# Kernel optimization log

Hardware: AMD Instinct MI355X
Metric: run time of the kernel (lower is better)

Reference implementation:

```python
import jax, jax.numpy as jnp
import numpy as np

NUM_ATOMS = 50000
NUM_EDGES = 200000  # even: edges come in (fwd, rev) pairs
D_V, D_E, D_H = 133, 14, 256
DEPTH = 3


def setup_inputs() -> dict:
    key = jax.random.key(0)
    ks = jax.random.split(key, 12)
    half = NUM_EDGES // 2
    src = jax.random.randint(ks[0], (half,), 0, NUM_ATOMS)
    dst = jax.random.randint(ks[1], (half,), 0, NUM_ATOMS)
    v = jnp.concatenate([src, dst])
    w = jnp.concatenate([dst, src])
    edge_index = jnp.stack([v, w])  # [2, E]
    rev_edge_index = jnp.concatenate([jnp.arange(half) + half, jnp.arange(half)])

    def lin(k, out_d, in_d):
        return jax.random.normal(k, (out_d, in_d), jnp.float32) / np.sqrt(in_d)

    return {
        "V": jax.random.normal(ks[2], (NUM_ATOMS, D_V), jnp.float32),
        "E_feat": jax.random.normal(ks[3], (NUM_EDGES, D_E), jnp.float32),
        "edge_index": edge_index,
        "rev_edge_index": rev_edge_index,
        "Wi_atom": lin(ks[4], D_H, D_V),
        "Wi_bond": lin(ks[5], D_H, D_V + D_E),
        "Wh_atom": lin(ks[6], D_H, D_H),
        "Wh_bond": lin(ks[7], D_H, D_H),
        "Wf_atom": lin(ks[8], D_H, D_H),
        "Wf_bond": lin(ks[9], D_H, D_H),
        "Wo_atom": lin(ks[10], D_H, D_V + D_H),
    }


def _sum_and_max_into_atoms(H_e, w_idx, num_atoms):
    a_sum = jax.ops.segment_sum(H_e, w_idx, num_segments=num_atoms)
    a_max = jax.ops.segment_max(H_e, w_idx, num_segments=num_atoms)
    a_max = jnp.where(jnp.isfinite(a_max), a_max, 0.0)  # empty segments -> 0
    return a_sum, a_max


def _fuse(H, m, Wf):
    # Fusion(kind='mlp', residual=True), dropout=0:
    # residual update with a small MLP on the combined signal
    return H + jax.nn.relu((H + m) @ Wf.T)


def reference(V, E_feat, edge_index, rev_edge_index, Wi_atom, Wi_bond,
              Wh_atom, Wh_bond, Wf_atom, Wf_bond, Wo_atom):
    tau = jax.nn.relu
    num_atoms = V.shape[0]
    v = edge_index[0]
    w = edge_index[1]

    H_a = tau(V @ Wi_atom.T)                                        # [N, d_h]
    H_b = tau(jnp.concatenate([V[v], E_feat], axis=1) @ Wi_bond.T)  # [E, d_h]

    for _ in range(1, DEPTH):
        a_sum, a_max = _sum_and_max_into_atoms(H_b, w, num_atoms)
        gate = a_sum * a_max
        m_a = gate @ Wh_atom.T
        H_a = _fuse(H_a, m_a, Wf_atom)

        M_b = a_sum[v] - H_b[rev_edge_index]
        m_b = M_b @ Wh_bond.T
        H_b = _fuse(H_b, m_b, Wf_bond)

    a_sum, _ = _sum_and_max_into_atoms(H_b, w, num_atoms)
    H_atom = tau(jnp.concatenate([V, a_sum], axis=1) @ Wo_atom.T)   # [N, d_h]
    return H_atom
```

## Files before the change

kernel.cpp:

```cpp
#include <hip/hip_runtime.h>
#include <hip/hip_bf16.h>

#define NATOM 50000
#define NEDGE 200000
#define HALF  100000
#define DV    133
#define DE    14
#define DH    256
#define KVP   160
#define NBLK_SCAN ((NATOM + 255) / 256)

typedef __bf16  bf16x8 __attribute__((ext_vector_type(8)));
typedef __bf16  bf16x4 __attribute__((ext_vector_type(4)));
typedef float   f32x4  __attribute__((ext_vector_type(4)));

__device__ __forceinline__ void gll16(const void* g, void* l) {
    __builtin_amdgcn_global_load_lds(
        (const __attribute__((address_space(1))) unsigned int*)g,
        (__attribute__((address_space(3))) unsigned int*)l, 16, 0, 0);
}
__device__ __forceinline__ void drain_barrier() {
    __builtin_amdgcn_s_waitcnt(0);
    __syncthreads();
}
__device__ __forceinline__ int swz(int row, int byteInRow) {
    return row * 512 + (byteInRow ^ ((row & 7) << 4));
}


struct DArgs {
    const float* Vf; const float* Ef; const float* asumf;
    const int* vidx;
    const __bf16* W1; const __bf16* W2;
    __bf16* C; float* Cf;
    int M;
};

template<int MODE, int KITERS>
__global__ __launch_bounds__(512, 4) void dgemm(DArgs g) {
    const int tid = threadIdx.x;
    const int lane = tid & 63, wv = tid >> 6;
    const int quad = lane >> 4, l16 = lane & 15;
    const int wr = (wv >> 2) * 64, wc = (wv & 3) * 64;
    const int gr0 = blockIdx.x * 128;

    int vrow[4]; const float* epp[4];
#pragma unroll
    for (int m = 0; m < 4; ++m) {
        int r = gr0 + wr + m * 16 + l16;
        if (r > g.M - 1) r = g.M - 1;
        vrow[m] = (MODE == 1) ? g.vidx[r] : r;
        epp[m] = (MODE == 1) ? (g.Ef + (size_t)r * DE) : nullptr;
    }

    f32x4 acc[16];
#pragma unroll
    for (int i = 0; i < 16; ++i) acc[i] = (f32x4){0.f, 0.f, 0.f, 0.f};

#pragma unroll
    for (int kk = 0; kk < KITERS; ++kk) {
        bf16x8 af[4];
#pragma unroll
        for (int m = 0; m < 4; ++m) {
            const int cb = kk * 32 + quad * 8;
            if (MODE != 2 || kk < 5) {
                const float* vp = g.Vf + (size_t)vrow[m] * DV;
                if (kk < 4) {
                    f32x4 x0, x1;
                    __builtin_memcpy(&x0, vp + cb, 16);
                    __builtin_memcpy(&x1, vp + cb + 4, 16);
#pragma unroll
                    for (int j = 0; j < 4; ++j) {
                        af[m][j] = (__bf16)x0[j]; af[m][4 + j] = (__bf16)x1[j];
                    }
                } else {
#pragma unroll
                    for (int j = 0; j < 8; ++j) {
                        int c = cb + j; float y = 0.f;
                        if (c < DV) y = vp[c];
                        else if (MODE == 1 && c < DV + DE) y = epp[m][c - DV];
                        af[m][j] = (__bf16)y;
                    }
                }
            } else {
                const float* sp = g.asumf + (size_t)vrow[m] * DH + (kk - 5) * 32 + quad * 8;
                f32x4 s0 = *(const f32x4*)sp, s1 = *(const f32x4*)(sp + 4);
#pragma unroll
                for (int j = 0; j < 4; ++j) {
                    af[m][j] = (__bf16)s0[j]; af[m][4 + j] = (__bf16)s1[j];
                }
            }
        }
        bf16x8 bfv[4];
#pragma unroll
        for (int n = 0; n < 4; ++n) {
            int col = wc + n * 16 + l16;
            const __bf16* wp;
            if (MODE == 2 && kk >= 5) wp = g.W2 + (size_t)col * DH  + (kk - 5) * 32 + quad * 8;
            else                      wp = g.W1 + (size_t)col * KVP + kk * 32 + quad * 8;
            bfv[n] = *(const bf16x8*)wp;
        }
#pragma unroll
        for (int m = 0; m < 4; ++m)
#pragma unroll
            for (int n = 0; n < 4; ++n)
                acc[m * 4 + n] = __builtin_amdgcn_mfma_f32_16x16x32_bf16(
                    af[m], bfv[n], acc[m * 4 + n], 0, 0, 0);
    }

#pragma unroll
    for (int m = 0; m < 4; ++m)
#pragma unroll
    for (int n = 0; n < 4; ++n)
#pragma unroll
    for (int r = 0; r < 4; ++r) {
        int gr = gr0 + wr + m * 16 + quad * 4 + r;
        if (gr < g.M) {
            int col = wc + n * 16 + l16;
            float v = acc[m * 4 + n][r];
            v = v > 0.f ? v : 0.f;
            if (MODE == 2) g.Cf[(size_t)gr * DH + col] = v;
            else           g.C [(size_t)gr * DH + col] = (__bf16)v;
        }
    }
}

struct FArgs {
    const float* asumf; const __bf16* asumb; const __bf16* amaxb;
    const int* vidx;
    const __bf16* W1; const __bf16* W2;
    __bf16* H;
    int M;
};

template<int BOND>
__global__ __launch_bounds__(512, 2) void fgemm(FArgs g) {
    __shared__ __bf16 Hlds[32768];
    __shared__ __bf16 Tlds[32768];
    const int tid = threadIdx.x;
    const int lane = tid & 63, wv = tid >> 6;
    const int quad = lane >> 4, l16 = lane & 15;
    const int wr = (wv >> 2) * 64, wc = (wv & 3) * 64;
    const int bid = blockIdx.x;

#pragma unroll
    for (int it = 0; it < 8; ++it) {
        int unit = it * 512 + wv * 64 + lane;
        int lr = unit >> 5, u16 = unit & 31;
        int srow;
        if (BOND) {
            int sl = bid * 64 + (lr & 63); if (sl > g.M - 1) sl = g.M - 1;
            srow = (lr < 64) ? sl : g.M + sl;
        } else {
            srow = bid * 128 + lr; if (srow > g.M - 1) srow = g.M - 1;
        }
        const char* src = (const char*)g.H + (size_t)srow * 512
                        + ((u16 * 16) ^ ((lr & 7) << 4));
        gll16(src, (char*)Hlds + it * 8192 + wv * 1024);
    }

    int garow[4];
#pragma unroll
    for (int m = 0; m < 4; ++m) {
        int lr = wr + m * 16 + l16;
        if (BOND) {
            int sl = bid * 64 + (lr & 63); if (sl > g.M - 1) sl = g.M - 1;
            int gA = (lr < 64) ? sl : g.M + sl;
            garow[m] = g.vidx[gA];
        } else {
            int r = bid * 128 + lr; if (r > g.M - 1) r = g.M - 1;
            garow[m] = r;
        }
    }

    f32x4 acc[16];
#pragma unroll
    for (int i = 0; i < 16; ++i) acc[i] = (f32x4){0.f, 0.f, 0.f, 0.f};

    drain_barrier();

#pragma unroll
    for (int kk = 0; kk < 8; ++kk) {
        const int cb = kk * 32 + quad * 8;
        const int byC = cb * 2;
        bf16x8 af[4];
#pragma unroll
        for (int m = 0; m < 4; ++m) {
            int lr = wr + m * 16 + l16;
            if (BOND) {
                bf16x8 a = *(const bf16x8*)(g.asumb + (size_t)garow[m] * DH + cb);
                int lrH = lr ^ 64;
                bf16x8 h = *(const bf16x8*)((const char*)Hlds + swz(lrH, byC));
#pragma unroll
                for (int j = 0; j < 8; ++j)
                    af[m][j] = (__bf16)((float)a[j] - (float)h[j]);
            } else {
                const float* s = g.asumf + (size_t)garow[m] * DH + cb;
                f32x4 s0 = *(const f32x4*)s, s1 = *(const f32x4*)(s + 4);
                bf16x8 mx = *(const bf16x8*)(g.amaxb + (size_t)garow[m] * DH + cb);
#pragma unroll
                for (int j = 0; j < 4; ++j) {
                    af[m][j]     = (__bf16)(s0[j] * (float)mx[j]);
                    af[m][4 + j] = (__bf16)(s1[j] * (float)mx[4 + j]);
                }
            }
        }
        bf16x8 bfv[4];
#pragma unroll
        for (int n = 0; n < 4; ++n)
            bfv[n] = *(const bf16x8*)(g.W1 + (size_t)(wc + n * 16 + l16) * DH + cb);
#pragma unroll
        for (int m = 0; m < 4; ++m)
#pragma unroll
            for (int n = 0; n < 4; ++n)
                acc[m * 4 + n] = __builtin_amdgcn_mfma_f32_16x16x32_bf16(
                    af[m], bfv[n], acc[m * 4 + n], 0, 0, 0);
    }

#pragma unroll
    for (int m = 0; m < 4; ++m)
#pragma unroll
    for (int n = 0; n < 4; ++n)
#pragma unroll
    for (int r = 0; r < 4; ++r) {
        int lr = wr + m * 16 + quad * 4 + r;
        int col = wc + n * 16 + l16;
        float b = (float)*(const __bf16*)((const char*)Hlds + swz(lr, col * 2));
        *(__bf16*)((char*)Tlds + swz(lr, col * 2)) = (__bf16)(b + acc[m * 4 + n][r]);
    }
    drain_barrier();

#pragma unroll
    for (int i = 0; i < 16; ++i) acc[i] = (f32x4){0.f, 0.f, 0.f, 0.f};
#pragma unroll
    for (int kk = 0; kk < 8; ++kk) {
        bf16x8 af[4], bfv[4];
#pragma unroll
        for (int m = 0; m < 4; ++m) {
            int lr = wr + m * 16 + l16;
            af[m] = *(const bf16x8*)((const char*)Tlds + swz(lr, kk * 64 + quad * 16));
        }
#pragma unroll
        for (int n = 0; n < 4; ++n)
            bfv[n] = *(const bf16x8*)(g.W2 + (size_t)(wc + n * 16 + l16) * DH + kk * 32 + quad * 8);
#pragma unroll
        for (int m = 0; m < 4; ++m)
#pragma unroll
            for (int n = 0; n < 4; ++n)
                acc[m * 4 + n] = __builtin_amdgcn_mfma_f32_16x16x32_bf16(
                    af[m], bfv[n], acc[m * 4 + n], 0, 0, 0);
    }

#pragma unroll
    for (int m = 0; m < 4; ++m)
#pragma unroll
    for (int n = 0; n < 4; ++n)
#pragma unroll
    for (int r = 0; r < 4; ++r) {
        int lr = wr + m * 16 + quad * 4 + r;
        int col = wc + n * 16 + l16;
        int off = swz(lr, col * 2);
        float b = (float)*(const __bf16*)((const char*)Hlds + off);
        float v = acc[m * 4 + n][r];
        v = v > 0.f ? v : 0.f;
        *(__bf16*)((char*)Hlds + off) = (__bf16)(b + v);
    }
    drain_barrier();

#pragma unroll
    for (int it = 0; it < 8; ++it) {
        int unit = it * 512 + tid;
        int lr = unit >> 5, u16 = unit & 31;
        bool ok; int srow;
        if (BOND) {
            int sl = bid * 64 + (lr & 63); ok = sl < g.M;
            srow = (lr < 64) ? sl : g.M + sl;
        } else {
            srow = bid * 128 + lr; ok = srow < g.M;
        }
        if (ok) {
            bf16x8 v = *(const bf16x8*)((const char*)Hlds
                        + swz(lr, u16 * 16));
            *(bf16x8*)((char*)g.H + (size_t)srow * 512 + u16 * 16) = v;
        }
    }
}

__global__ void count_deg(const int* __restrict__ widx, int* __restrict__ cnt) {
    int e = blockIdx.x * 256 + threadIdx.x;
    if (e < NEDGE) atomicAdd(&cnt[widx[e]], 1);
}

__global__ __launch_bounds__(256) void scan_p1(const int* __restrict__ cnt,
                                               int* __restrict__ rowptr,
                                               int* __restrict__ bsum) {
    __shared__ int sm[256];
    const int tid = threadIdx.x;
    const int i = blockIdx.x * 256 + tid;
    int v = (i < NATOM) ? cnt[i] : 0;
    sm[tid] = v;
    __syncthreads();
    for (int off = 1; off < 256; off <<= 1) {
        int t = (tid >= off) ? sm[tid - off] : 0;
        __syncthreads();
        sm[tid] += t;
        __syncthreads();
    }
    if (i < NATOM) rowptr[i] = sm[tid] - v;
    if (tid == 255) bsum[blockIdx.x] = sm[255];
}

__global__ __launch_bounds__(256) void scan_p2(int* __restrict__ bsum) {
    __shared__ int sm[256];
    const int tid = threadIdx.x;
    int v = (tid < NBLK_SCAN) ? bsum[tid] : 0;
    sm[tid] = v;
    __syncthreads();
    for (int off = 1; off < 256; off <<= 1) {
        int t = (tid >= off) ? sm[tid - off] : 0;
        __syncthreads();
        sm[tid] += t;
        __syncthreads();
    }
    if (tid < NBLK_SCAN) bsum[tid] = sm[tid] - v;
    if (tid == 255) bsum[NBLK_SCAN] = sm[255];
}

__global__ __launch_bounds__(256) void scan_p3(int* __restrict__ rowptr,
                                               int* __restrict__ cursor,
                                               const int* __restrict__ bsum) {
    const int i = blockIdx.x * 256 + threadIdx.x;
    if (i < NATOM) {
        int r = rowptr[i] + bsum[blockIdx.x];
        rowptr[i] = r;
        cursor[i] = r;
    }
    if (i == 0) rowptr[NATOM] = bsum[NBLK_SCAN];
}

__global__ void fill_csr(const int* __restrict__ widx, int* __restrict__ cursor,
                         int* __restrict__ eid) {
    int e = blockIdx.x * 256 + threadIdx.x;
    if (e >= NEDGE) return;
    int pos = atomicAdd(&cursor[widx[e]], 1);
    eid[pos] = e;
}

template<int WITHMAX>
__global__ __launch_bounds__(256) void seg_reduce(
    const __bf16* __restrict__ Hb, const int* __restrict__ rowptr,
    const int* __restrict__ eid,
    float* __restrict__ asum, __bf16* __restrict__ asumb,
    __bf16* __restrict__ amaxb)
{
    int a = blockIdx.x * 4 + (threadIdx.x >> 6);
    if (a >= NATOM) return;
    const int lane = threadIdx.x & 63;
    const int beg = rowptr[a], end = rowptr[a + 1];
    float s0 = 0.f, s1 = 0.f, s2 = 0.f, s3 = 0.f;
    float m0 = 0.f, m1 = 0.f, m2 = 0.f, m3 = 0.f;
    for (int i = beg; i < end; ++i) {
        int e = eid[i];
        bf16x4 h = *(const bf16x4*)(Hb + (size_t)e * DH + lane * 4);
        float v0 = (float)h[0], v1 = (float)h[1], v2 = (float)h[2], v3 = (float)h[3];
        s0 += v0; s1 += v1; s2 += v2; s3 += v3;
        if (WITHMAX) {
            m0 = fmaxf(m0, v0); m1 = fmaxf(m1, v1);
            m2 = fmaxf(m2, v2); m3 = fmaxf(m3, v3);
        }
    }
    size_t o = (size_t)a * DH + lane * 4;
    *(f32x4*)(asum + o) = (f32x4){s0, s1, s2, s3};
    if (WITHMAX) {
        bf16x4 sv; sv[0] = (__bf16)s0; sv[1] = (__bf16)s1; sv[2] = (__bf16)s2; sv[3] = (__bf16)s3;
        *(bf16x4*)(asumb + o) = sv;
        bf16x4 mv; mv[0] = (__bf16)m0; mv[1] = (__bf16)m1; mv[2] = (__bf16)m2; mv[3] = (__bf16)m3;
        *(bf16x4*)(amaxb + o) = mv;
    }
}

__global__ void pad_w2(const float* __restrict__ src, __bf16* __restrict__ dst,
                       int srcld, int coloff, int KS, int KD) {
    int i = blockIdx.x * 256 + threadIdx.x;
    if (i >= 256 * KD) return;
    int n = i / KD, c = i - n * KD;
    dst[i] = (c < KS) ? (__bf16)src[(size_t)n * srcld + coloff + c] : (__bf16)0.f;
}

static inline int cdiv(long a, long b) { return (int)((a + b - 1) / b); }

extern "C" void kernel_launch(void* const* d_in, const int* in_sizes, int n_in,
                              void* d_out, int out_size, void* d_ws, size_t ws_size,
                              hipStream_t stream) {
    const float* V    = (const float*)d_in[0];
    const float* Ef   = (const float*)d_in[1];
    const int*   ei   = (const int*)d_in[2];
    const int*   rev  = (const int*)d_in[3];
    const float* Wi_a = (const float*)d_in[4];
    const float* Wi_b = (const float*)d_in[5];
    const float* Wh_a = (const float*)d_in[6];
    const float* Wh_b = (const float*)d_in[7];
    const float* Wf_a = (const float*)d_in[8];
    const float* Wf_b = (const float*)d_in[9];
    const float* Wo   = (const float*)d_in[10];
    float* out = (float*)d_out;
    (void)rev;

    const int* vidx = ei;
    const int* widx = ei + NEDGE;

    char* ws = (char*)d_ws;
    __bf16* Hb    = (__bf16*)(ws + 0);
    __bf16* Ha    = (__bf16*)(ws + 102400000);
    float*  asum  = (float*) (ws + 128000000);
    __bf16* asumb = (__bf16*)(ws + 179200000);
    __bf16* amaxb = (__bf16*)(ws + 204800000);
    __bf16* Wia   = (__bf16*)(ws + 230400000);
    __bf16* Wib   = (__bf16*)(ws + 230481920);
    __bf16* Wo1   = (__bf16*)(ws + 230563840);
    __bf16* Wo2   = (__bf16*)(ws + 230645760);
    __bf16* Wha   = (__bf16*)(ws + 230776832);
    __bf16* Whb   = (__bf16*)(ws + 230907904);
    __bf16* Wfa   = (__bf16*)(ws + 231038976);
    __bf16* Wfb   = (__bf16*)(ws + 231170048);
    int*  rowptr  = (int*)(ws + 231301120);
    int*  cursor  = (int*)(ws + 231501312);
    int*  eid     = (int*)(ws + 231701504);
    int*  bsum    = (int*)(ws + 232501504);
    (void)ws_size;

    hipMemsetAsync(cursor, 0, NATOM * sizeof(int), stream);
    count_deg<<<cdiv(NEDGE, 256), 256, 0, stream>>>(widx, cursor);
    scan_p1<<<NBLK_SCAN, 256, 0, stream>>>(cursor, rowptr, bsum);
    scan_p2<<<1, 256, 0, stream>>>(bsum);
    scan_p3<<<NBLK_SCAN, 256, 0, stream>>>(rowptr, cursor, bsum);
    fill_csr<<<cdiv(NEDGE, 256), 256, 0, stream>>>(widx, cursor, eid);

    pad_w2<<<cdiv(256 * KVP, 256), 256, 0, stream>>>(Wi_a, Wia, DV, 0, DV, KVP);
    pad_w2<<<cdiv(256 * KVP, 256), 256, 0, stream>>>(Wi_b, Wib, DV + DE, 0, DV + DE, KVP);
    pad_w2<<<cdiv(256 * KVP, 256), 256, 0, stream>>>(Wo, Wo1, DV + DH, 0, DV, KVP);
    pad_w2<<<cdiv(256 * DH, 256), 256, 0, stream>>>(Wo, Wo2, DV + DH, DV, DH, DH);
    pad_w2<<<cdiv(256 * DH, 256), 256, 0, stream>>>(Wh_a, Wha, DH, 0, DH, DH);
    pad_w2<<<cdiv(256 * DH, 256), 256, 0, stream>>>(Wh_b, Whb, DH, 0, DH, DH);
    pad_w2<<<cdiv(256 * DH, 256), 256, 0, stream>>>(Wf_a, Wfa, DH, 0, DH, DH);
    pad_w2<<<cdiv(256 * DH, 256), 256, 0, stream>>>(Wf_b, Wfb, DH, 0, DH, DH);

    {
        DArgs d{}; d.Vf = V; d.W1 = Wia; d.C = Ha; d.M = NATOM;
        dgemm<0, 5><<<cdiv(NATOM, 128), 512, 0, stream>>>(d);
    }
    {
        DArgs d{}; d.Vf = V; d.Ef = Ef; d.vidx = vidx; d.W1 = Wib; d.C = Hb; d.M = NEDGE;
        dgemm<1, 5><<<cdiv(NEDGE, 128), 512, 0, stream>>>(d);
    }

    for (int it = 0; it < 2; ++it) {
        seg_reduce<1><<<cdiv(NATOM, 4), 256, 0, stream>>>(Hb, rowptr, eid, asum, asumb, amaxb);
        {
            FArgs f{}; f.asumf = asum; f.amaxb = amaxb;
            f.W1 = Wha; f.W2 = Wfa; f.H = Ha; f.M = NATOM;
            fgemm<0><<<cdiv(NATOM, 128), 512, 0, stream>>>(f);
        }
        {
            FArgs f{}; f.asumb = asumb; f.vidx = vidx;
            f.W1 = Whb; f.W2 = Wfb; f.H = Hb; f.M = HALF;
            fgemm<1><<<cdiv(HALF, 64), 512, 0, stream>>>(f);
        }
    }

    seg_reduce<0><<<cdiv(NATOM, 4), 256, 0, stream>>>(Hb, rowptr, eid, asum, nullptr, nullptr);
    {
        DArgs d{}; d.Vf = V; d.asumf = asum; d.W1 = Wo1; d.W2 = Wo2; d.Cf = out; d.M = NATOM;
        dgemm<2, 13><<<cdiv(NATOM, 128), 512, 0, stream>>>(d);
    }
}
```

Before: 1.089 ms.

## Halve fgemm row tile, swap MFMA operands, prefetch gathered asum rows

```diff
diff --git a/kernel.cpp b/kernel.cpp
--- a/kernel.cpp
+++ b/kernel.cpp
@@ -134,153 +134,158 @@
 };
 
 template<int BOND>
-__global__ __launch_bounds__(512, 2) void fgemm(FArgs g) {
-    __shared__ __bf16 Hlds[32768];
-    __shared__ __bf16 Tlds[32768];
+__global__ __launch_bounds__(512, 4) void fgemm(FArgs g) {
+    __shared__ __bf16 Hlds[16384];
+    __shared__ __bf16 Tlds[16384];
     const int tid = threadIdx.x;
     const int lane = tid & 63, wv = tid >> 6;
     const int quad = lane >> 4, l16 = lane & 15;
-    const int wr = (wv >> 2) * 64, wc = (wv & 3) * 64;
+    const int wr = (wv >> 2) * 32;
+    const int wc = (wv & 3) * 64;
     const int bid = blockIdx.x;
 
-#pragma unroll
-    for (int it = 0; it < 8; ++it) {
+    int garow[2];
+#pragma unroll
+    for (int fr = 0; fr < 2; ++fr) {
+        int lr = wr + fr * 16 + l16;
+        if (BOND) {
+            int sl = bid * 32 + (lr & 31);
+            int gA = (lr < 32) ? sl : HALF + sl;
+            garow[fr] = g.vidx[gA];
+        } else {
+            int r = bid * 64 + lr; if (r > g.M - 1) r = g.M - 1;
+            garow[fr] = r;
+        }
+    }
+    bf16x8 pf[2][8];
+    if (BOND) {
+#pragma unroll
+        for (int fr = 0; fr < 2; ++fr)
+#pragma unroll
+        for (int kk = 0; kk < 8; ++kk)
+            pf[fr][kk] = *(const bf16x8*)(g.asumb + (size_t)garow[fr] * DH
+                                          + kk * 32 + quad * 8);
+    }
+
+#pragma unroll
+    for (int it = 0; it < 4; ++it) {
         int unit = it * 512 + wv * 64 + lane;
         int lr = unit >> 5, u16 = unit & 31;
         int srow;
-        if (BOND) {
-            int sl = bid * 64 + (lr & 63); if (sl > g.M - 1) sl = g.M - 1;
-            srow = (lr < 64) ? sl : g.M + sl;
-        } else {
-            srow = bid * 128 + lr; if (srow > g.M - 1) srow = g.M - 1;
-        }
+        if (BOND) { int sl = bid * 32 + (lr & 31); srow = (lr < 32) ? sl : HALF + sl; }
+        else      { srow = bid * 64 + lr; if (srow > g.M - 1) srow = g.M - 1; }
         const char* src = (const char*)g.H + (size_t)srow * 512
                         + ((u16 * 16) ^ ((lr & 7) << 4));
         gll16(src, (char*)Hlds + it * 8192 + wv * 1024);
     }
-
-    int garow[4];
-#pragma unroll
-    for (int m = 0; m < 4; ++m) {
-        int lr = wr + m * 16 + l16;
-        if (BOND) {
-            int sl = bid * 64 + (lr & 63); if (sl > g.M - 1) sl = g.M - 1;
-            int gA = (lr < 64) ? sl : g.M + sl;
-            garow[m] = g.vidx[gA];
-        } else {
-            int r = bid * 128 + lr; if (r > g.M - 1) r = g.M - 1;
-            garow[m] = r;
-        }
-    }
-
-    f32x4 acc[16];
-#pragma unroll
-    for (int i = 0; i < 16; ++i) acc[i] = (f32x4){0.f, 0.f, 0.f, 0.f};
-
     drain_barrier();
+
+    f32x4 acc[8];
+#pragma unroll
+    for (int i = 0; i < 8; ++i) acc[i] = (f32x4){0.f, 0.f, 0.f, 0.f};
 
 #pragma unroll
     for (int kk = 0; kk < 8; ++kk) {
         const int cb = kk * 32 + quad * 8;
-        const int byC = cb * 2;
-        bf16x8 af[4];
-#pragma unroll
-        for (int m = 0; m < 4; ++m) {
-            int lr = wr + m * 16 + l16;
+        bf16x8 mf[2];
+#pragma unroll
+        for (int fr = 0; fr < 2; ++fr) {
+            int lr = wr + fr * 16 + l16;
             if (BOND) {
-                bf16x8 a = *(const bf16x8*)(g.asumb + (size_t)garow[m] * DH + cb);
-                int lrH = lr ^ 64;
-                bf16x8 h = *(const bf16x8*)((const char*)Hlds + swz(lrH, byC));
+                bf16x8 h = *(const bf16x8*)((const char*)Hlds + swz(lr ^ 32, cb * 2));
 #pragma unroll
                 for (int j = 0; j < 8; ++j)
-                    af[m][j] = (__bf16)((float)a[j] - (float)h[j]);
+                    mf[fr][j] = (__bf16)((float)pf[fr][kk][j] - (float)h[j]);
             } else {
-                const float* s = g.asumf + (size_t)garow[m] * DH + cb;
+                const float* s = g.asumf + (size_t)garow[fr] * DH + cb;
                 f32x4 s0 = *(const f32x4*)s, s1 = *(const f32x4*)(s + 4);
-                bf16x8 mx = *(const bf16x8*)(g.amaxb + (size_t)garow[m] * DH + cb);
+                bf16x8 mx = *(const bf16x8*)(g.amaxb + (size_t)garow[fr] * DH + cb);
 #pragma unroll
                 for (int j = 0; j < 4; ++j) {
-                    af[m][j]     = (__bf16)(s0[j] * (float)mx[j]);
-                    af[m][4 + j] = (__bf16)(s1[j] * (float)mx[4 + j]);
+                    mf[fr][j]     = (__bf16)(s0[j] * (float)mx[j]);
+                    mf[fr][4 + j] = (__bf16)(s1[j] * (float)mx[4 + j]);
                 }
             }
         }
-        bf16x8 bfv[4];
-#pragma unroll
-        for (int n = 0; n < 4; ++n)
-            bfv[n] = *(const bf16x8*)(g.W1 + (size_t)(wc + n * 16 + l16) * DH + cb);
-#pragma unroll
-        for (int m = 0; m < 4; ++m)
-#pragma unroll
-            for (int n = 0; n < 4; ++n)
-                acc[m * 4 + n] = __builtin_amdgcn_mfma_f32_16x16x32_bf16(
-                    af[m], bfv[n], acc[m * 4 + n], 0, 0, 0);
-    }
-
-#pragma unroll
-    for (int m = 0; m < 4; ++m)
-#pragma unroll
-    for (int n = 0; n < 4; ++n)
-#pragma unroll
-    for (int r = 0; r < 4; ++r) {
-        int lr = wr + m * 16 + quad * 4 + r;
-        int col = wc + n * 16 + l16;
-        float b = (float)*(const __bf16*)((const char*)Hlds + swz(lr, col * 2));
-        *(__bf16*)((char*)Tlds + swz(lr, col * 2)) = (__bf16)(b + acc[m * 4 + n][r]);
+        bf16x8 wf[4];
+#pragma unroll
+        for (int fc = 0; fc < 4; ++fc)
+            wf[fc] = *(const bf16x8*)(g.W1 + (size_t)(wc + fc * 16 + l16) * DH + cb);
+#pragma unroll
+        for (int fc = 0; fc < 4; ++fc)
+#pragma unroll
+            for (int fr = 0; fr < 2; ++fr)
+                acc[fc * 2 + fr] = __builtin_amdgcn_mfma_f32_16x16x32_bf16(
+                    wf[fc], mf[fr], acc[fc * 2 + fr], 0, 0, 0);
+    }
+
+#pragma unroll
+    for (int fc = 0; fc < 4; ++fc)
+#pragma unroll
+    for (int fr = 0; fr < 2; ++fr) {
+        int row = wr + fr * 16 + l16;
+        int colb = wc + fc * 16 + quad * 4;
+        int off = swz(row, colb * 2);
+        bf16x4 h = *(const bf16x4*)((const char*)Hlds + off);
+        bf16x4 t;
+#pragma unroll
+        for (int j = 0; j < 4; ++j)
+            t[j] = (__bf16)((float)h[j] + acc[fc * 2 + fr][j]);
+        *(bf16x4*)((char*)Tlds + off) = t;
     }
     drain_barrier();
 
 #pragma unroll
-    for (int i = 0; i < 16; ++i) acc[i] = (f32x4){0.f, 0.f, 0.f, 0.f};
+    for (int i = 0; i < 8; ++i) acc[i] = (f32x4){0.f, 0.f, 0.f, 0.f};
 #pragma unroll
     for (int kk = 0; kk < 8; ++kk) {
-        bf16x8 af[4], bfv[4];
-#pragma unroll
-        for (int m = 0; m < 4; ++m) {
-            int lr = wr + m * 16 + l16;
-            af[m] = *(const bf16x8*)((const char*)Tlds + swz(lr, kk * 64 + quad * 16));
-        }
-#pragma unroll
-        for (int n = 0; n < 4; ++n)
-            bfv[n] = *(const bf16x8*)(g.W2 + (size_t)(wc + n * 16 + l16) * DH + kk * 32 + quad * 8);
-#pragma unroll
-        for (int m = 0; m < 4; ++m)
-#pragma unroll
-            for (int n = 0; n < 4; ++n)
-                acc[m * 4 + n] = __builtin_amdgcn_mfma_f32_16x16x32_bf16(
-                    af[m], bfv[n], acc[m * 4 + n], 0, 0, 0);
-    }
-
-#pragma unroll
-    for (int m = 0; m < 4; ++m)
-#pragma unroll
-    for (int n = 0; n < 4; ++n)
-#pragma unroll
-    for (int r = 0; r < 4; ++r) {
-        int lr = wr + m * 16 + quad * 4 + r;
-        int col = wc + n * 16 + l16;
-        int off = swz(lr, col * 2);
-        float b = (float)*(const __bf16*)((const char*)Hlds + off);
-        float v = acc[m * 4 + n][r];
-        v = v > 0.f ? v : 0.f;
-        *(__bf16*)((char*)Hlds + off) = (__bf16)(b + v);
+        const int cb = kk * 32 + quad * 8;
+        bf16x8 tf[2];
+#pragma unroll
+        for (int fr = 0; fr < 2; ++fr) {
+            int lr = wr + fr * 16 + l16;
+            tf[fr] = *(const bf16x8*)((const char*)Tlds + swz(lr, cb * 2));
+        }
+        bf16x8 wf[4];
+#pragma unroll
+        for (int fc = 0; fc < 4; ++fc)
+            wf[fc] = *(const bf16x8*)(g.W2 + (size_t)(wc + fc * 16 + l16) * DH + cb);
+#pragma unroll
+        for (int fc = 0; fc < 4; ++fc)
+#pragma unroll
+            for (int fr = 0; fr < 2; ++fr)
+                acc[fc * 2 + fr] = __builtin_amdgcn_mfma_f32_16x16x32_bf16(
+                    wf[fc], tf[fr], acc[fc * 2 + fr], 0, 0, 0);
+    }
+
+#pragma unroll
+    for (int fc = 0; fc < 4; ++fc)
+#pragma unroll
+    for (int fr = 0; fr < 2; ++fr) {
+        int row = wr + fr * 16 + l16;
+        int colb = wc + fc * 16 + quad * 4;
+        int off = swz(row, colb * 2);
+        bf16x4 h = *(const bf16x4*)((const char*)Hlds + off);
+        bf16x4 o;
+#pragma unroll
+        for (int j = 0; j < 4; ++j) {
+            float v = acc[fc * 2 + fr][j];
+            v = v > 0.f ? v : 0.f;
+            o[j] = (__bf16)((float)h[j] + v);
+        }
+        *(bf16x4*)((char*)Hlds + off) = o;
     }
     drain_barrier();
 
 #pragma unroll
-    for (int it = 0; it < 8; ++it) {
+    for (int it = 0; it < 4; ++it) {
         int unit = it * 512 + tid;
         int lr = unit >> 5, u16 = unit & 31;
         bool ok; int srow;
-        if (BOND) {
-            int sl = bid * 64 + (lr & 63); ok = sl < g.M;
-            srow = (lr < 64) ? sl : g.M + sl;
-        } else {
-            srow = bid * 128 + lr; ok = srow < g.M;
-        }
+        if (BOND) { int sl = bid * 32 + (lr & 31); ok = true; srow = (lr < 32) ? sl : HALF + sl; }
+        else      { srow = bid * 64 + lr; ok = srow < g.M; }
         if (ok) {
-            bf16x8 v = *(const bf16x8*)((const char*)Hlds
-                        + swz(lr, u16 * 16));
+            bf16x8 v = *(const bf16x8*)((const char*)Hlds + swz(lr, u16 * 16));
             *(bf16x8*)((char*)g.H + (size_t)srow * 512 + u16 * 16) = v;
         }
     }
@@ -459,12 +464,12 @@
         {
             FArgs f{}; f.asumf = asum; f.amaxb = amaxb;
             f.W1 = Wha; f.W2 = Wfa; f.H = Ha; f.M = NATOM;
-            fgemm<0><<<cdiv(NATOM, 128), 512, 0, stream>>>(f);
+            fgemm<0><<<cdiv(NATOM, 64), 512, 0, stream>>>(f);
         }
         {
             FArgs f{}; f.asumb = asumb; f.vidx = vidx;
             f.W1 = Whb; f.W2 = Wfb; f.H = Hb; f.M = HALF;
-            fgemm<1><<<cdiv(HALF, 64), 512, 0, stream>>>(f);
+            fgemm<1><<<HALF / 32, 512, 0, stream>>>(f);
         }
     }
 
```

After: 1.224 ms. +12.4%, slower.
